# Kernel tuning notes

Hardware: AMD Instinct MI355X
Metric: run time of the kernel (lower is better)

Reference implementation:

```python
import jax, jax.numpy as jnp
import numpy as np

EMB = 1024
NHEAD = 16
HEAD_DIM = EMB // NHEAD  # 64
L = 2048
NEG = -1e30


def setup_inputs() -> dict:
    key = jax.random.key(0)
    ks = jax.random.split(key, 8)
    # xavier_uniform bound for square [EMB, EMB] matrices
    bound = float(np.sqrt(6.0 / (EMB + EMB)))
    def xavier(k):
        return jax.random.uniform(k, (EMB, EMB), jnp.float32, -bound, bound)
    return {
        "q": jax.random.normal(ks[0], (L, EMB), jnp.float32),
        "k": jax.random.normal(ks[1], (L, EMB), jnp.float32),
        "v": jax.random.normal(ks[2], (L, EMB), jnp.float32),
        "mask": jax.random.randint(ks[3], (NHEAD, L, L), 0, 2) > 0,
        "Wq": xavier(ks[4]),
        "Wk": xavier(ks[5]),
        "Wv": xavier(ks[6]),
        "Wo": xavier(ks[7]),
    }


def reference(q, k, v, mask, Wq, Wk, Wv, Wo):
    scaling = HEAD_DIM ** -0.5
    # F.linear(x, W) = x @ W.T ; reshape to [H, L, D]
    Q = (q @ Wq.T).reshape(L, NHEAD, HEAD_DIM).swapaxes(0, 1)
    K = (k @ Wk.T).reshape(L, NHEAD, HEAD_DIM).swapaxes(0, 1)
    V = (v @ Wv.T).reshape(L, NHEAD, HEAD_DIM).swapaxes(0, 1)
    scores = jnp.einsum("hld,hmd->hlm", Q, K) * scaling  # [H, L, L]
    scores = jnp.where(mask, jnp.asarray(NEG, scores.dtype), scores)
    p = jax.nn.softmax(scores, axis=-1)
    # attn_mask=True: multiplicative re-mask after softmax (custom path)
    p = p * (~mask).astype(p.dtype)
    # dropout is a no-op in eval mode
    attn_out = jnp.einsum("hlm,hmd->hld", p, V)  # [H, L, D]
    attn_out = attn_out.swapaxes(0, 1).reshape(L, EMB)
    return attn_out @ Wo.T
```

## Files before the change

kernel.cpp:

```cpp
#include <hip/hip_runtime.h>
#include <stdint.h>

#define EMB   1024
#define NHEAD 16
#define HDIM  64
#define SEQ   2048

typedef unsigned short ushort_t;
typedef unsigned int   uint32;
typedef __attribute__((ext_vector_type(8))) short bfrag;
typedef __attribute__((ext_vector_type(4))) float ffrag;

#define MFMA(a, b, c) __builtin_amdgcn_mfma_f32_16x16x32_bf16((a), (b), (c), 0, 0, 0)

__device__ inline ushort_t f2bf(float f) {
  uint32 u = __float_as_uint(f);
  u += 0x7FFFu + ((u >> 16) & 1u);
  return (ushort_t)(u >> 16);
}
__device__ inline uint32 pack2(float a, float b) {
  return (uint32)f2bf(a) | ((uint32)f2bf(b) << 16);
}

__device__ inline void glds16(const ushort_t* g, ushort_t* l) {
  __builtin_amdgcn_global_load_lds(
      (const __attribute__((address_space(1))) uint32*)(uintptr_t)g,
      (__attribute__((address_space(3))) uint32*)(uintptr_t)l, 16, 0, 0);
}

__global__ void detect_mask_kernel(const uint32* __restrict__ mw, int* __restrict__ flag) {
  uint32 w = mw[threadIdx.x];
  bool is4 = (w == 0u) || (w == 1u) || (w == 0x3F800000u);
  unsigned long long bad = __ballot(!is4);
  if (threadIdx.x == 0) flag[0] = (bad == 0ull) ? 1 : 0;
}

__global__ __launch_bounds__(256) void compress_mask(
    const void* __restrict__ maskp, const int* __restrict__ flag, ushort_t* __restrict__ bm)
{
  size_t t = (size_t)blockIdx.x * 256 + threadIdx.x;
  size_t row = t >> 7;
  int c16 = (int)(t & 127);
  size_t base = row * SEQ + (size_t)c16 * 16;
  ushort_t mv = 0;
  if (*flag) {
    const uint4* p = (const uint4*)((const uint32*)maskp + base);
    uint4 a0 = p[0], a1 = p[1], a2 = p[2], a3 = p[3];
    uint32 aw[16] = {a0.x,a0.y,a0.z,a0.w, a1.x,a1.y,a1.z,a1.w,
                     a2.x,a2.y,a2.z,a2.w, a3.x,a3.y,a3.z,a3.w};
    #pragma unroll
    for (int i = 0; i < 16; ++i) mv |= (ushort_t)((aw[i] != 0u) ? 1u : 0u) << i;
  } else {
    uint4 b0 = *(const uint4*)((const unsigned char*)maskp + base);
    uint32 bw[4] = {b0.x, b0.y, b0.z, b0.w};
    #pragma unroll
    for (int i = 0; i < 16; ++i)
      mv |= (ushort_t)((((bw[i >> 2] >> ((i & 3) * 8)) & 0xFFu) != 0u) ? 1u : 0u) << i;
  }
  bm[t] = mv;
}

__global__ __launch_bounds__(256) void cvt_all(
    const float4* __restrict__ q,  const float4* __restrict__ k,  const float4* __restrict__ v,
    const float4* __restrict__ wq, const float4* __restrict__ wk, const float4* __restrict__ wv,
    const float4* __restrict__ wo,
    uint2* __restrict__ qb,  uint2* __restrict__ kb,  uint2* __restrict__ vb,
    uint2* __restrict__ wqb, uint2* __restrict__ wkb, uint2* __restrict__ wvb,
    uint2* __restrict__ wob)
{
  int t = blockIdx.x * 256 + threadIdx.x;
  int s = blockIdx.y;
  const float4* src; uint2* dst; int n4;
  switch (s) {
    case 0: src = q;  dst = qb;  n4 = (SEQ * EMB) / 4; break;
    case 1: src = k;  dst = kb;  n4 = (SEQ * EMB) / 4; break;
    case 2: src = v;  dst = vb;  n4 = (SEQ * EMB) / 4; break;
    case 3: src = wq; dst = wqb; n4 = (EMB * EMB) / 4; break;
    case 4: src = wk; dst = wkb; n4 = (EMB * EMB) / 4; break;
    case 5: src = wv; dst = wvb; n4 = (EMB * EMB) / 4; break;
    default: src = wo; dst = wob; n4 = (EMB * EMB) / 4; break;
  }
  if (t >= n4) return;
  float4 f = src[t];
  uint2 o; o.x = pack2(f.x, f.y); o.y = pack2(f.z, f.w);
  dst[t] = o;
}

template<int MODE, int BN>
__device__ inline void gemm_body(const ushort_t* A, const ushort_t* B, void* Cp,
                                 int m0, int n0, ushort_t* As, ushort_t* Bs) {
  const int tid = threadIdx.x, lane = tid & 63, w = tid >> 6;
  const int wm = (w >> 1) * 64, wn = (w & 1) * (BN / 2);
  const int col = lane & 15, g = lane >> 4;
  constexpr int TN = BN / 32;
  constexpr int BIT = BN / 32;

  ffrag acc[4][TN] = {};

  for (int k0 = 0; k0 < EMB; k0 += 64) {
    __syncthreads();
    #pragma unroll
    for (int it = 0; it < 4; ++it) {
      int p = it * 256 + tid;
      int row = p >> 3, pc = p & 7;
      glds16(A + (size_t)(m0 + row) * EMB + k0 + (pc ^ (row & 7)) * 8, &As[p * 8]);
    }
    #pragma unroll
    for (int it = 0; it < BIT; ++it) {
      int p = it * 256 + tid;
      int row = p >> 3, pc = p & 7;
      glds16(B + (size_t)(n0 + row) * EMB + k0 + (pc ^ (row & 7)) * 8, &Bs[p * 8]);
    }
    __syncthreads();

    #pragma unroll
    for (int c = 0; c < 2; ++c) {
      bfrag av[4], bv[TN];
      #pragma unroll
      for (int t = 0; t < 4; ++t) {
        int ra = wm + t * 16 + col;
        av[t] = *(const bfrag*)&As[ra * 64 + ((c * 4 + g) ^ (ra & 7)) * 8];
      }
      #pragma unroll
      for (int t = 0; t < TN; ++t) {
        int rb = wn + t * 16 + col;
        bv[t] = *(const bfrag*)&Bs[rb * 64 + ((c * 4 + g) ^ (rb & 7)) * 8];
      }
      #pragma unroll
      for (int tm = 0; tm < 4; ++tm)
        #pragma unroll
        for (int tn = 0; tn < TN; ++tn)
          acc[tm][tn] = MFMA(av[tm], bv[tn], acc[tm][tn]);
    }
  }

  const int rbase = g * 4;
  #pragma unroll
  for (int tm = 0; tm < 4; ++tm)
    #pragma unroll
    for (int tn = 0; tn < TN; ++tn)
      #pragma unroll
      for (int r = 0; r < 4; ++r) {
        int m = m0 + wm + tm * 16 + rbase + r;
        int n = n0 + wn + tn * 16 + col;
        float vv = acc[tm][tn][r];
        if (MODE == 0) {
          ((ushort_t*)Cp)[((size_t)(n >> 6) * SEQ + m) * HDIM + (n & 63)] = f2bf(vv);
        } else if (MODE == 1) {
          ((ushort_t*)Cp)[((size_t)(m >> 6) * HDIM + (m & 63)) * SEQ + n] = f2bf(vv);
        } else {
          ((float*)Cp)[(size_t)m * EMB + n] = vv;
        }
      }
}

__global__ __launch_bounds__(256) void gemm_qkv(
    const ushort_t* __restrict__ qb, const ushort_t* __restrict__ kb, const ushort_t* __restrict__ vb,
    const ushort_t* __restrict__ Wqb, const ushort_t* __restrict__ Wkb, const ushort_t* __restrict__ Wvb,
    ushort_t* __restrict__ Qb, ushort_t* __restrict__ Kb, ushort_t* __restrict__ Vtb)
{
  __shared__ ushort_t As[128 * 64];
  __shared__ ushort_t Bs[64 * 64];
  const int z = blockIdx.y, bid = blockIdx.x;
  if (z == 0) {
    gemm_body<0, 64>(qb, Wqb, Qb, (bid >> 4) * 128, (bid & 15) * 64, As, Bs);
  } else if (z == 1) {
    gemm_body<0, 64>(kb, Wkb, Kb, (bid >> 4) * 128, (bid & 15) * 64, As, Bs);
  } else {
    gemm_body<1, 64>(Wvb, vb, Vtb, (bid >> 5) * 128, (bid & 31) * 64, As, Bs);
  }
}

__global__ __launch_bounds__(256) void gemm_out(
    const ushort_t* __restrict__ A, const ushort_t* __restrict__ B, float* __restrict__ C)
{
  __shared__ ushort_t As[128 * 64];
  __shared__ ushort_t Bs[64 * 64];
  gemm_body<2, 64>(A, B, (void*)C, blockIdx.y * 128, blockIdx.x * 64, As, Bs);
}

__global__ __launch_bounds__(256) void attn_mfma(
    const ushort_t* __restrict__ Qb,
    const ushort_t* __restrict__ Kb,
    const ushort_t* __restrict__ Vtb,
    const ushort_t* __restrict__ bm,
    ushort_t* __restrict__ attnb)
{
  __shared__ ushort_t KVs[2][2][64 * 64];
  __shared__ ushort_t Ps[4][16 * 72];

  const int tid  = threadIdx.x;
  const int lane = tid & 63;
  const int w    = tid >> 6;
  const int h    = blockIdx.y;
  const int l0   = blockIdx.x * 64;
  const int col  = lane & 15, g = lane >> 4, kg8 = g * 8, rbase = g * 4;

  ushort_t* pw = &Ps[w][0];

  {
    int rl = lane >> 2, seg = (lane & 3) * 16;
    const uint4* pq = (const uint4*)(Qb + ((size_t)h * SEQ + l0 + w * 16 + rl) * HDIM + seg);
    uint4 q0 = pq[0], q1 = pq[1];
    *(uint4*)&pw[rl * 72 + seg] = q0;
    *(uint4*)&pw[rl * 72 + seg + 8] = q1;
  }
  bfrag qf[2];
  qf[0] = *(const bfrag*)&pw[col * 72 + kg8];
  qf[1] = *(const bfrag*)&pw[col * 72 + 32 + kg8];

  auto stage_kv = [&](int kt_, int buf) {
    #pragma unroll
    for (int it = 0; it < 2; ++it) {
      int p = it * 256 + tid;
      int row = p >> 3, pc = p & 7;
      int sc = (pc ^ (row & 7)) * 8;
      glds16(Kb + ((size_t)h * SEQ + kt_ + row) * HDIM + sc, &KVs[buf][0][p * 8]);
      glds16(Vtb + ((size_t)h * HDIM + row) * SEQ + kt_ + sc, &KVs[buf][1][p * 8]);
    }
  };
  stage_kv(0, 0);

  const size_t bmbase = ((size_t)h * SEQ + l0 + w * 16 + (lane >> 2)) * 128 + (lane & 3);
  ushort_t mv_next = bm[bmbase];

  float lsum[4] = {0.f, 0.f, 0.f, 0.f};
  ffrag oacc[4] = {};

  for (int t = 0; t < 32; ++t) {
    const int buf = t & 1;
    __syncthreads();
    stage_kv(((t + 1) & 31) * 64, buf ^ 1);

    const ushort_t* Kc = &KVs[buf][0][0];
    const ushort_t* Vc = &KVs[buf][1][0];

    ushort_t mv = mv_next;
    mv_next = bm[bmbase + ((t + 1) & 31) * 4];

    ffrag s[4] = {};
    #pragma unroll
    for (int c = 0; c < 2; ++c)
      #pragma unroll
      for (int tn = 0; tn < 4; ++tn) {
        int row = tn * 16 + col;
        bfrag kf = *(const bfrag*)&Kc[row * 64 + ((c * 4 + g) ^ (row & 7)) * 8];
        s[tn] = MFMA(qf[c], kf, s[tn]);
      }

    #pragma unroll
    for (int r = 0; r < 4; ++r) {
      #pragma unroll
      for (int tn = 0; tn < 4; ++tn) {
        int m16 = __shfl((int)mv, (rbase + r) * 4 + tn, 64);
        bool msk = ((m16 >> col) & 1) != 0;
        float x = s[tn][r] * 0.125f;
        float p = msk ? 0.f : __expf(x);
        lsum[r] += p;
        pw[(rbase + r) * 72 + tn * 16 + col] = f2bf(p);
      }
    }

    #pragma unroll
    for (int c = 0; c < 2; ++c) {
      bfrag af = *(const bfrag*)&pw[col * 72 + c * 32 + kg8];
      #pragma unroll
      for (int tn = 0; tn < 4; ++tn) {
        int row = tn * 16 + col;
        bfrag vf = *(const bfrag*)&Vc[row * 64 + ((c * 4 + g) ^ (row & 7)) * 8];
        oacc[tn] = MFMA(af, vf, oacc[tn]);
      }
    }
  }

  float inv[4];
  #pragma unroll
  for (int r = 0; r < 4; ++r) {
    float s_ = lsum[r];
    #pragma unroll
    for (int off = 1; off < 16; off <<= 1) s_ += __shfl_xor(s_, off, 64);
    inv[r] = (s_ > 0.f) ? (1.0f / s_) : 0.0f;
  }
  #pragma unroll
  for (int tn = 0; tn < 4; ++tn)
    #pragma unroll
    for (int r = 0; r < 4; ++r) {
      int qg = l0 + w * 16 + rbase + r;
      attnb[(size_t)qg * EMB + h * HDIM + tn * 16 + col] = f2bf(oacc[tn][r] * inv[r]);
    }
}

extern "C" void kernel_launch(void* const* d_in, const int* in_sizes, int n_in,
                              void* d_out, int out_size, void* d_ws, size_t ws_size,
                              hipStream_t stream) {
  const float* q    = (const float*)d_in[0];
  const float* k    = (const float*)d_in[1];
  const float* v    = (const float*)d_in[2];
  const void*  mask =               d_in[3];
  const float* Wq   = (const float*)d_in[4];
  const float* Wk   = (const float*)d_in[5];
  const float* Wv   = (const float*)d_in[6];
  const float* Wo   = (const float*)d_in[7];

  char* ws = (char*)d_ws;
  const size_t MB = 1024 * 1024;
  ushort_t* qb    = (ushort_t*)(ws);
  ushort_t* kb    = (ushort_t*)(ws + 4  * MB);
  ushort_t* vb    = (ushort_t*)(ws + 8  * MB);
  ushort_t* Wqb   = (ushort_t*)(ws + 12 * MB);
  ushort_t* Wkb   = (ushort_t*)(ws + 14 * MB);
  ushort_t* Wvb   = (ushort_t*)(ws + 16 * MB);
  ushort_t* Wob   = (ushort_t*)(ws + 18 * MB);
  ushort_t* Qb    = (ushort_t*)(ws + 20 * MB);
  ushort_t* Kb    = (ushort_t*)(ws + 24 * MB);
  ushort_t* Vtb   = (ushort_t*)(ws + 28 * MB);
  int*      flag  = (int*)     (ws + 32 * MB);
  ushort_t* bmask = (ushort_t*)(ws + 33 * MB);
  ushort_t* attnb = qb;

  detect_mask_kernel<<<1, 64, 0, stream>>>((const uint32*)mask, flag);

  compress_mask<<<16384, 256, 0, stream>>>(mask, flag, bmask);

  cvt_all<<<dim3((SEQ * EMB / 4 + 255) / 256, 7), 256, 0, stream>>>(
      (const float4*)q, (const float4*)k, (const float4*)v,
      (const float4*)Wq, (const float4*)Wk, (const float4*)Wv, (const float4*)Wo,
      (uint2*)qb, (uint2*)kb, (uint2*)vb,
      (uint2*)Wqb, (uint2*)Wkb, (uint2*)Wvb, (uint2*)Wob);

  gemm_qkv<<<dim3(256, 3), 256, 0, stream>>>(qb, kb, vb, Wqb, Wkb, Wvb, Qb, Kb, Vtb);

  attn_mfma<<<dim3(SEQ / 64, NHEAD), 256, 0, stream>>>(Qb, Kb, Vtb, bmask, attnb);

  gemm_out<<<dim3(16, 16), 256, 0, stream>>>(attnb, Wob, (float*)d_out);
}
```

Baseline: 482.3 us.

## Double-buffer GEMM tiles and restructure attention loop with transposed scores

The projection GEMMs now double-buffer their A/B LDS tiles, so the next K slice is fetched while the current one is multiplied, at the cost of twice the shared memory. The attention kernel processes 128 keys per iteration, split into two 64-key halves. It computes transposed score tiles (K as the A operand), so each lane owns a query column and can pack P values as vectorized stores, and the row-sum collapses to a cross-group reduction. K is double-buffered while V is single-buffered and reloaded after a barrier. The mask bits are read in a transposed layout to match.

```diff
diff --git a/kernel.cpp b/kernel.cpp
--- a/kernel.cpp
+++ b/kernel.cpp
@@ -94,24 +94,38 @@
   const int col = lane & 15, g = lane >> 4;
   constexpr int TN = BN / 32;
   constexpr int BIT = BN / 32;
+  constexpr int ASZ = 128 * 64;
+  constexpr int BSZ = BN * 64;
 
   ffrag acc[4][TN] = {};
 
-  for (int k0 = 0; k0 < EMB; k0 += 64) {
-    __syncthreads();
+  auto stage = [&](int kt, int buf) {
+    const int k0 = kt * 64;
+    ushort_t* Ad = As + buf * ASZ;
+    ushort_t* Bd = Bs + buf * BSZ;
     #pragma unroll
     for (int it = 0; it < 4; ++it) {
       int p = it * 256 + tid;
       int row = p >> 3, pc = p & 7;
-      glds16(A + (size_t)(m0 + row) * EMB + k0 + (pc ^ (row & 7)) * 8, &As[p * 8]);
+      glds16(A + (size_t)(m0 + row) * EMB + k0 + (pc ^ (row & 7)) * 8, &Ad[p * 8]);
     }
     #pragma unroll
     for (int it = 0; it < BIT; ++it) {
       int p = it * 256 + tid;
       int row = p >> 3, pc = p & 7;
-      glds16(B + (size_t)(n0 + row) * EMB + k0 + (pc ^ (row & 7)) * 8, &Bs[p * 8]);
-    }
+      glds16(B + (size_t)(n0 + row) * EMB + k0 + (pc ^ (row & 7)) * 8, &Bd[p * 8]);
+    }
+  };
+
+  stage(0, 0);
+
+  for (int kt = 0; kt < 16; ++kt) {
+    const int buf = kt & 1;
     __syncthreads();
+    if (kt < 15) stage(kt + 1, buf ^ 1);
+
+    const ushort_t* Ac = As + buf * ASZ;
+    const ushort_t* Bc = Bs + buf * BSZ;
 
     #pragma unroll
     for (int c = 0; c < 2; ++c) {
@@ -119,12 +133,12 @@
       #pragma unroll
       for (int t = 0; t < 4; ++t) {
         int ra = wm + t * 16 + col;
-        av[t] = *(const bfrag*)&As[ra * 64 + ((c * 4 + g) ^ (ra & 7)) * 8];
+        av[t] = *(const bfrag*)&Ac[ra * 64 + ((c * 4 + g) ^ (ra & 7)) * 8];
       }
       #pragma unroll
       for (int t = 0; t < TN; ++t) {
         int rb = wn + t * 16 + col;
-        bv[t] = *(const bfrag*)&Bs[rb * 64 + ((c * 4 + g) ^ (rb & 7)) * 8];
+        bv[t] = *(const bfrag*)&Bc[rb * 64 + ((c * 4 + g) ^ (rb & 7)) * 8];
       }
       #pragma unroll
       for (int tm = 0; tm < 4; ++tm)
@@ -159,8 +173,8 @@
     const ushort_t* __restrict__ Wqb, const ushort_t* __restrict__ Wkb, const ushort_t* __restrict__ Wvb,
     ushort_t* __restrict__ Qb, ushort_t* __restrict__ Kb, ushort_t* __restrict__ Vtb)
 {
-  __shared__ ushort_t As[128 * 64];
-  __shared__ ushort_t Bs[64 * 64];
+  __shared__ ushort_t As[2 * 128 * 64];
+  __shared__ ushort_t Bs[2 * 64 * 64];
   const int z = blockIdx.y, bid = blockIdx.x;
   if (z == 0) {
     gemm_body<0, 64>(qb, Wqb, Qb, (bid >> 4) * 128, (bid & 15) * 64, As, Bs);
@@ -174,8 +188,8 @@
 __global__ __launch_bounds__(256) void gemm_out(
     const ushort_t* __restrict__ A, const ushort_t* __restrict__ B, float* __restrict__ C)
 {
-  __shared__ ushort_t As[128 * 64];
-  __shared__ ushort_t Bs[64 * 64];
+  __shared__ ushort_t As[2 * 128 * 64];
+  __shared__ ushort_t Bs[2 * 64 * 64];
   gemm_body<2, 64>(A, B, (void*)C, blockIdx.y * 128, blockIdx.x * 64, As, Bs);
 }
 
@@ -186,7 +200,8 @@
     const ushort_t* __restrict__ bm,
     ushort_t* __restrict__ attnb)
 {
-  __shared__ ushort_t KVs[2][2][64 * 64];
+  __shared__ ushort_t Ks[2][2][64 * 64];
+  __shared__ ushort_t Vs[2][64 * 64];
   __shared__ ushort_t Ps[4][16 * 72];
 
   const int tid  = threadIdx.x;
@@ -209,57 +224,76 @@
   qf[0] = *(const bfrag*)&pw[col * 72 + kg8];
   qf[1] = *(const bfrag*)&pw[col * 72 + 32 + kg8];
 
-  auto stage_kv = [&](int kt_, int buf) {
+  auto stage_k = [&](int t2, int buf) {
+    const int cb = t2 * 128;
     #pragma unroll
     for (int it = 0; it < 2; ++it) {
       int p = it * 256 + tid;
       int row = p >> 3, pc = p & 7;
       int sc = (pc ^ (row & 7)) * 8;
-      glds16(Kb + ((size_t)h * SEQ + kt_ + row) * HDIM + sc, &KVs[buf][0][p * 8]);
-      glds16(Vtb + ((size_t)h * HDIM + row) * SEQ + kt_ + sc, &KVs[buf][1][p * 8]);
+      glds16(Kb + ((size_t)h * SEQ + cb + row) * HDIM + sc,      &Ks[buf][0][p * 8]);
+      glds16(Kb + ((size_t)h * SEQ + cb + 64 + row) * HDIM + sc, &Ks[buf][1][p * 8]);
     }
   };
-  stage_kv(0, 0);
-
-  const size_t bmbase = ((size_t)h * SEQ + l0 + w * 16 + (lane >> 2)) * 128 + (lane & 3);
-  ushort_t mv_next = bm[bmbase];
-
-  float lsum[4] = {0.f, 0.f, 0.f, 0.f};
+  auto stage_v = [&](int t2) {
+    const int cb = t2 * 128;
+    #pragma unroll
+    for (int it = 0; it < 2; ++it) {
+      int p = it * 256 + tid;
+      int row = p >> 3, pc = p & 7;
+      int sc = (pc ^ (row & 7)) * 8;
+      glds16(Vtb + ((size_t)h * HDIM + row) * SEQ + cb + sc,      &Vs[0][p * 8]);
+      glds16(Vtb + ((size_t)h * HDIM + row) * SEQ + cb + 64 + sc, &Vs[1][p * 8]);
+    }
+  };
+
+  stage_k(0, 0);
+  stage_v(0);
+  __syncthreads();
+
+  const size_t bmbase = ((size_t)h * SEQ + l0 + w * 16 + col) * 128 + g;
+  ushort_t mvn0 = bm[bmbase];
+  ushort_t mvn1 = bm[bmbase + 4];
+
+  float lsum = 0.f;
   ffrag oacc[4] = {};
 
-  for (int t = 0; t < 32; ++t) {
+  for (int t = 0; t < 16; ++t) {
     const int buf = t & 1;
-    __syncthreads();
-    stage_kv(((t + 1) & 31) * 64, buf ^ 1);
-
-    const ushort_t* Kc = &KVs[buf][0][0];
-    const ushort_t* Vc = &KVs[buf][1][0];
-
-    ushort_t mv = mv_next;
-    mv_next = bm[bmbase + ((t + 1) & 31) * 4];
-
-    ffrag s[4] = {};
+    if (t < 15) stage_k(t + 1, buf ^ 1);
+
+    int mv0 = (int)mvn0, mv1 = (int)mvn1;
+    if (t < 15) {
+      mvn0 = bm[bmbase + (size_t)(t + 1) * 8];
+      mvn1 = bm[bmbase + (size_t)(t + 1) * 8 + 4];
+    }
+
+    ffrag s0[4] = {}, s1[4] = {};
     #pragma unroll
     for (int c = 0; c < 2; ++c)
       #pragma unroll
       for (int tn = 0; tn < 4; ++tn) {
         int row = tn * 16 + col;
-        bfrag kf = *(const bfrag*)&Kc[row * 64 + ((c * 4 + g) ^ (row & 7)) * 8];
-        s[tn] = MFMA(qf[c], kf, s[tn]);
-      }
-
-    #pragma unroll
-    for (int r = 0; r < 4; ++r) {
-      #pragma unroll
-      for (int tn = 0; tn < 4; ++tn) {
-        int m16 = __shfl((int)mv, (rbase + r) * 4 + tn, 64);
-        bool msk = ((m16 >> col) & 1) != 0;
-        float x = s[tn][r] * 0.125f;
-        float p = msk ? 0.f : __expf(x);
-        lsum[r] += p;
-        pw[(rbase + r) * 72 + tn * 16 + col] = f2bf(p);
-      }
-    }
+        int sw = ((c * 4 + g) ^ (row & 7)) * 8;
+        bfrag kf0 = *(const bfrag*)&Ks[buf][0][row * 64 + sw];
+        bfrag kf1 = *(const bfrag*)&Ks[buf][1][row * 64 + sw];
+        s0[tn] = MFMA(kf0, qf[c], s0[tn]);
+        s1[tn] = MFMA(kf1, qf[c], s1[tn]);
+      }
+
+    #pragma unroll
+    for (int tn = 0; tn < 4; ++tn) {
+      int m16 = __shfl(mv0, tn * 16 + col, 64);
+      float p0 = ((m16 >> (rbase + 0)) & 1) ? 0.f : __expf(s0[tn][0] * 0.125f);
+      float p1 = ((m16 >> (rbase + 1)) & 1) ? 0.f : __expf(s0[tn][1] * 0.125f);
+      float p2 = ((m16 >> (rbase + 2)) & 1) ? 0.f : __expf(s0[tn][2] * 0.125f);
+      float p3 = ((m16 >> (rbase + 3)) & 1) ? 0.f : __expf(s0[tn][3] * 0.125f);
+      lsum += (p0 + p1) + (p2 + p3);
+      uint2 pk; pk.x = pack2(p0, p1); pk.y = pack2(p2, p3);
+      *(uint2*)&pw[col * 72 + tn * 16 + rbase] = pk;
+    }
+
+    __syncthreads();
 
     #pragma unroll
     for (int c = 0; c < 2; ++c) {
@@ -267,20 +301,46 @@
       #pragma unroll
       for (int tn = 0; tn < 4; ++tn) {
         int row = tn * 16 + col;
-        bfrag vf = *(const bfrag*)&Vc[row * 64 + ((c * 4 + g) ^ (row & 7)) * 8];
+        bfrag vf = *(const bfrag*)&Vs[0][row * 64 + ((c * 4 + g) ^ (row & 7)) * 8];
         oacc[tn] = MFMA(af, vf, oacc[tn]);
       }
     }
-  }
-
+
+    #pragma unroll
+    for (int tn = 0; tn < 4; ++tn) {
+      int m16 = __shfl(mv1, tn * 16 + col, 64);
+      float p0 = ((m16 >> (rbase + 0)) & 1) ? 0.f : __expf(s1[tn][0] * 0.125f);
+      float p1 = ((m16 >> (rbase + 1)) & 1) ? 0.f : __expf(s1[tn][1] * 0.125f);
+      float p2 = ((m16 >> (rbase + 2)) & 1) ? 0.f : __expf(s1[tn][2] * 0.125f);
+      float p3 = ((m16 >> (rbase + 3)) & 1) ? 0.f : __expf(s1[tn][3] * 0.125f);
+      lsum += (p0 + p1) + (p2 + p3);
+      uint2 pk; pk.x = pack2(p0, p1); pk.y = pack2(p2, p3);
+      *(uint2*)&pw[col * 72 + tn * 16 + rbase] = pk;
+    }
+
+    #pragma unroll
+    for (int c = 0; c < 2; ++c) {
+      bfrag af = *(const bfrag*)&pw[col * 72 + c * 32 + kg8];
+      #pragma unroll
+      for (int tn = 0; tn < 4; ++tn) {
+        int row = tn * 16 + col;
+        bfrag vf = *(const bfrag*)&Vs[1][row * 64 + ((c * 4 + g) ^ (row & 7)) * 8];
+        oacc[tn] = MFMA(af, vf, oacc[tn]);
+      }
+    }
+
+    __syncthreads();
+    if (t < 15) stage_v(t + 1);
+  }
+
+  float s_ = lsum;
+  s_ += __shfl_xor(s_, 16, 64);
+  s_ += __shfl_xor(s_, 32, 64);
+  float invf = (s_ > 0.f) ? (1.0f / s_) : 0.0f;
   float inv[4];
   #pragma unroll
-  for (int r = 0; r < 4; ++r) {
-    float s_ = lsum[r];
-    #pragma unroll
-    for (int off = 1; off < 16; off <<= 1) s_ += __shfl_xor(s_, off, 64);
-    inv[r] = (s_ > 0.f) ? (1.0f / s_) : 0.0f;
-  }
+  for (int r = 0; r < 4; ++r) inv[r] = __shfl(invf, rbase + r, 64);
+
   #pragma unroll
   for (int tn = 0; tn < 4; ++tn)
     #pragma unroll
```

Measured after the change: 468.9 us. 1.03x faster.
